# Optimization experiments

Hardware: AMD Instinct MI355X
Metric: run time of the kernel (lower is better)

Reference implementation:

```python
import jax, jax.numpy as jnp
import numpy as np


def setup_inputs() -> dict:
    key = jax.random.key(0)
    ks = jax.random.split(key, 10)
    B, S, V, E, C = 256, 512, 50000, 300, 10
    sentences = jax.random.randint(ks[0], (B, S), 0, V)
    emb_table = jax.random.normal(ks[1], (V, E), dtype=jnp.float32) * 0.1
    # pad_token=0 row zeroed like nn.Embedding(padding_idx=0)
    emb_table = emb_table.at[0].set(0.0)
    k3 = jax.random.normal(ks[2], (3, E), dtype=jnp.float32) * 0.05
    b3 = jax.random.normal(ks[3], (1,), dtype=jnp.float32) * 0.05
    k4 = jax.random.normal(ks[4], (4, E), dtype=jnp.float32) * 0.05
    b4 = jax.random.normal(ks[5], (1,), dtype=jnp.float32) * 0.05
    k5 = jax.random.normal(ks[6], (5, E), dtype=jnp.float32) * 0.05
    b5 = jax.random.normal(ks[7], (1,), dtype=jnp.float32) * 0.05
    fc_w = jax.random.normal(ks[8], (C, 3), dtype=jnp.float32) * 0.1
    fc_b = jax.random.normal(ks[9], (C,), dtype=jnp.float32) * 0.1
    return {"sentences": sentences, "emb_table": emb_table,
            "k3": k3, "b3": b3, "k4": k4, "b4": b4, "k5": k5, "b5": b5,
            "fc_w": fc_w, "fc_b": fc_b}


def _window_feature(emb, k, b):
    # emb: [B,S,E]; k: [w,E]; conv with 1 in/1 out channel spanning full E (VALID)
    out = jax.lax.conv_general_dilated(
        emb[:, None, :, :],            # [B,1,S,E]
        k[None, None, :, :],           # [1,1,w,E]
        window_strides=(1, 1), padding="VALID")  # [B,1,S-w+1,1]
    f = jnp.tanh(out[:, 0, :, 0] + b)  # [B,S-w+1]
    return f.max(axis=-1)              # [B]


def reference(sentences, emb_table, k3, b3, k4, b4, k5, b5, fc_w, fc_b):
    emb = emb_table[sentences]  # [B,S,E]
    feats = jnp.stack([_window_feature(emb, k3, b3),
                       _window_feature(emb, k4, b4),
                       _window_feature(emb, k5, b5)], axis=-1)  # [B,3]
    # dropout is identity in eval mode
    logits = feats @ fc_w.T + fc_b  # [B,C]
    return jax.nn.log_softmax(logits, axis=-1)
```

## Files before the change

### kernel.cpp

```cpp
#include <hip/hip_runtime.h>
#include <math.h>

#define NSENT 256
#define SLEN  512
#define VROWS 50000
#define EDIM  300
#define NC4   75
#define NROW  12

__global__ __launch_bounds__(256, 4)
void vocab_scores(const float* __restrict__ emb,
                  const float* __restrict__ k3,
                  const float* __restrict__ k4,
                  const float* __restrict__ k5,
                  float* __restrict__ s)
{
    __shared__ float part[4][64][13];
    __shared__ float red[64 * 13];

    const int lane  = threadIdx.x & 63;
    const int wave  = threadIdx.x >> 6;
    const int chunk = __builtin_amdgcn_readfirstlane(wave);

    const int v0 = blockIdx.x * 64;
    const int v  = min(v0 + lane, VROWS - 1);

    const float4* erow = reinterpret_cast<const float4*>(emb + (size_t)v * EDIM);
    const float4* k3v  = reinterpret_cast<const float4*>(k3);
    const float4* k4v  = reinterpret_cast<const float4*>(k4);
    const float4* k5v  = reinterpret_cast<const float4*>(k5);

    const int  c0   = chunk * 19;
    const bool full = (chunk < 3);

    float4 ev[18];
    #pragma unroll
    for (int i = 0; i < 18; ++i) ev[i] = erow[c0 + i];
    float4 evL;
    if (full) evL = erow[c0 + 18];

    float acc[NROW];
    #pragma unroll
    for (int r = 0; r < NROW; ++r) acc[r] = 0.f;

    auto fma_col = [&](const float4 ev_, int c) {
        #pragma unroll
        for (int r = 0; r < 3; ++r) {
            const float4 kv = k3v[r * NC4 + c];
            acc[r] = fmaf(ev_.x, kv.x, acc[r]);
            acc[r] = fmaf(ev_.y, kv.y, acc[r]);
            acc[r] = fmaf(ev_.z, kv.z, acc[r]);
            acc[r] = fmaf(ev_.w, kv.w, acc[r]);
        }
        #pragma unroll
        for (int r = 0; r < 4; ++r) {
            const float4 kv = k4v[r * NC4 + c];
            acc[3+r] = fmaf(ev_.x, kv.x, acc[3+r]);
            acc[3+r] = fmaf(ev_.y, kv.y, acc[3+r]);
            acc[3+r] = fmaf(ev_.z, kv.z, acc[3+r]);
            acc[3+r] = fmaf(ev_.w, kv.w, acc[3+r]);
        }
        #pragma unroll
        for (int r = 0; r < 5; ++r) {
            const float4 kv = k5v[r * NC4 + c];
            acc[7+r] = fmaf(ev_.x, kv.x, acc[7+r]);
            acc[7+r] = fmaf(ev_.y, kv.y, acc[7+r]);
            acc[7+r] = fmaf(ev_.z, kv.z, acc[7+r]);
            acc[7+r] = fmaf(ev_.w, kv.w, acc[7+r]);
        }
    };

    #pragma unroll
    for (int i = 0; i < 18; ++i) fma_col(ev[i], c0 + i);
    if (full) fma_col(evL, c0 + 18);

    #pragma unroll
    for (int r = 0; r < NROW; ++r) part[wave][lane][r] = acc[r];
    __syncthreads();

    const int r0 = wave * 3;
    #pragma unroll
    for (int rr = 0; rr < 3; ++rr) {
        const int r = r0 + rr;
        red[lane * 13 + r] = part[0][lane][r] + part[1][lane][r] +
                             part[2][lane][r] + part[3][lane][r];
    }
    __syncthreads();

    for (int j = threadIdx.x; j < 64 * NROW; j += 256) {
        const int gi = v0 * NROW + j;
        if (gi < VROWS * NROW)
            s[gi] = red[(j / NROW) * 13 + (j % NROW)];
    }
}

__global__ __launch_bounds__(1024, 1)
void textcnn_finish(const int*   __restrict__ sent,
                    const float* __restrict__ s,
                    const float* __restrict__ b3,
                    const float* __restrict__ b4,
                    const float* __restrict__ b5,
                    const float* __restrict__ fcw,
                    const float* __restrict__ fcb,
                    float* __restrict__ out)
{
    __shared__ float s_lds[NROW * SLEN];
    __shared__ float red[8][3];

    const int b = blockIdx.x;
    const int t = threadIdx.x;

    auto gather = [&](int token, int j) {
        const int widx = sent[b * SLEN + token];
        const float4 v = reinterpret_cast<const float4*>(s + (size_t)widx * NROW)[j];
        s_lds[(4*j + 0) * SLEN + token] = v.x;
        s_lds[(4*j + 1) * SLEN + token] = v.y;
        s_lds[(4*j + 2) * SLEN + token] = v.z;
        s_lds[(4*j + 3) * SLEN + token] = v.w;
    };

    gather(t & 511, t >> 9);
    if (t < SLEN) gather(t, 2);
    __syncthreads();

    if (t < SLEN) {
        const float bb3 = b3[0], bb4 = b4[0], bb5 = b5[0];
        float m3 = -1e30f, m4 = -1e30f, m5 = -1e30f;
        if (t < SLEN - 2)
            m3 = tanhf(s_lds[0*SLEN + t] + s_lds[1*SLEN + t+1] +
                       s_lds[2*SLEN + t+2] + bb3);
        if (t < SLEN - 3)
            m4 = tanhf(s_lds[3*SLEN + t] + s_lds[4*SLEN + t+1] +
                       s_lds[5*SLEN + t+2] + s_lds[6*SLEN + t+3] + bb4);
        if (t < SLEN - 4)
            m5 = tanhf(s_lds[7*SLEN + t] + s_lds[8*SLEN + t+1] +
                       s_lds[9*SLEN + t+2] + s_lds[10*SLEN + t+3] +
                       s_lds[11*SLEN + t+4] + bb5);

        #pragma unroll
        for (int off = 32; off; off >>= 1) {
            m3 = fmaxf(m3, __shfl_xor(m3, off));
            m4 = fmaxf(m4, __shfl_xor(m4, off));
            m5 = fmaxf(m5, __shfl_xor(m5, off));
        }
        if ((t & 63) == 0) {
            const int w = t >> 6;
            red[w][0] = m3; red[w][1] = m4; red[w][2] = m5;
        }
    }
    __syncthreads();

    if (t == 0) {
        float f3 = red[0][0], f4 = red[0][1], f5 = red[0][2];
        #pragma unroll
        for (int w = 1; w < 8; ++w) {
            f3 = fmaxf(f3, red[w][0]);
            f4 = fmaxf(f4, red[w][1]);
            f5 = fmaxf(f5, red[w][2]);
        }
        float lg[10];
        float mx = -1e30f;
        #pragma unroll
        for (int c = 0; c < 10; ++c) {
            lg[c] = fcb[c] + f3 * fcw[c*3+0] + f4 * fcw[c*3+1] + f5 * fcw[c*3+2];
            mx = fmaxf(mx, lg[c]);
        }
        float ssum = 0.f;
        #pragma unroll
        for (int c = 0; c < 10; ++c) ssum += expf(lg[c] - mx);
        const float lse = logf(ssum);
        #pragma unroll
        for (int c = 0; c < 10; ++c) out[b * 10 + c] = lg[c] - mx - lse;
    }
}

extern "C" void kernel_launch(void* const* d_in, const int* in_sizes, int n_in,
                              void* d_out, int out_size, void* d_ws, size_t ws_size,
                              hipStream_t stream) {
    const int*   sent = (const int*)  d_in[0];
    const float* emb  = (const float*)d_in[1];
    const float* k3   = (const float*)d_in[2];
    const float* b3   = (const float*)d_in[3];
    const float* k4   = (const float*)d_in[4];
    const float* b4   = (const float*)d_in[5];
    const float* k5   = (const float*)d_in[6];
    const float* b5   = (const float*)d_in[7];
    const float* fcw  = (const float*)d_in[8];
    const float* fcb  = (const float*)d_in[9];
    float* out = (float*)d_out;
    float* s   = (float*)d_ws;

    const int nblk = (VROWS + 63) / 64;
    vocab_scores<<<nblk, 256, 0, stream>>>(emb, k3, k4, k5, s);
    textcnn_finish<<<NSENT, 1024, 0, stream>>>(sent, s, b3, b4, b5, fcw, fcb, out);
}
```

Baseline: 28.44 us.

## Stage embedding tiles through LDS with coalesced loads and register prefetch

The vocab scoring kernel now loads each 64-row embedding tile with coalesced float4 loads across the whole block and writes it into a padded LDS buffer. Each lane then reads its row back from LDS for the dot products; before, every lane read its own row directly with strided global loads. Each block now handles two tiles, and the second tile's global loads are issued into registers before the first tile is computed, so the fetch overlaps the math. The cost is roughly 85KB of LDS per block and launch bounds of one block per CU, with half as many blocks. This lowers occupancy and may limit latency hiding on a memory-bound kernel.

```diff
diff --git a/kernel.cpp b/kernel.cpp
--- a/kernel.cpp
+++ b/kernel.cpp
@@ -7,91 +7,123 @@
 #define EDIM  300
 #define NC4   75
 #define NROW  12
-
-__global__ __launch_bounds__(256, 4)
+#define TROWS 64
+#define TF4   (TROWS * NC4)
+#define LDS_S4 77
+
+__global__ __launch_bounds__(256, 1)
 void vocab_scores(const float* __restrict__ emb,
                   const float* __restrict__ k3,
                   const float* __restrict__ k4,
                   const float* __restrict__ k5,
                   float* __restrict__ s)
 {
-    __shared__ float part[4][64][13];
-    __shared__ float red[64 * 13];
-
-    const int lane  = threadIdx.x & 63;
-    const int wave  = threadIdx.x >> 6;
+    __shared__ float4 ebuf[TROWS * LDS_S4];
+    __shared__ float  part[4][TROWS][13];
+    __shared__ float  red[TROWS * 13];
+
+    const int tid   = threadIdx.x;
+    const int lane  = tid & 63;
+    const int wave  = tid >> 6;
     const int chunk = __builtin_amdgcn_readfirstlane(wave);
-
-    const int v0 = blockIdx.x * 64;
-    const int v  = min(v0 + lane, VROWS - 1);
-
-    const float4* erow = reinterpret_cast<const float4*>(emb + (size_t)v * EDIM);
-    const float4* k3v  = reinterpret_cast<const float4*>(k3);
-    const float4* k4v  = reinterpret_cast<const float4*>(k4);
-    const float4* k5v  = reinterpret_cast<const float4*>(k5);
-
-    const int  c0   = chunk * 19;
+    const int c0    = chunk * 19;
     const bool full = (chunk < 3);
 
-    float4 ev[18];
-    #pragma unroll
-    for (int i = 0; i < 18; ++i) ev[i] = erow[c0 + i];
-    float4 evL;
-    if (full) evL = erow[c0 + 18];
-
-    float acc[NROW];
-    #pragma unroll
-    for (int r = 0; r < NROW; ++r) acc[r] = 0.f;
-
-    auto fma_col = [&](const float4 ev_, int c) {
+    const float4* embf4 = reinterpret_cast<const float4*>(emb);
+    const float4* k3v   = reinterpret_cast<const float4*>(k3);
+    const float4* k4v   = reinterpret_cast<const float4*>(k4);
+    const float4* k5v   = reinterpret_cast<const float4*>(k5);
+
+    const int row00 = blockIdx.x * (2 * TROWS);
+
+    float4 pre[19];
+
+    auto issue_loads = [&](int tile_row0) {
+        #pragma unroll
+        for (int k = 0; k < 19; ++k) {
+            const int g = k * 256 + tid;
+            float4 v = make_float4(0.f, 0.f, 0.f, 0.f);
+            if (g < TF4 && (tile_row0 + g / NC4) < VROWS)
+                v = embf4[tile_row0 * NC4 + g];
+            pre[k] = v;
+        }
+    };
+
+    auto write_lds = [&]() {
+        #pragma unroll
+        for (int k = 0; k < 19; ++k) {
+            const int g = k * 256 + tid;
+            if (g < TF4)
+                ebuf[(g / NC4) * LDS_S4 + (g % NC4)] = pre[k];
+        }
+    };
+
+    auto fma_col = [&](float acc[NROW], const float4 ev, int c) {
         #pragma unroll
         for (int r = 0; r < 3; ++r) {
             const float4 kv = k3v[r * NC4 + c];
-            acc[r] = fmaf(ev_.x, kv.x, acc[r]);
-            acc[r] = fmaf(ev_.y, kv.y, acc[r]);
-            acc[r] = fmaf(ev_.z, kv.z, acc[r]);
-            acc[r] = fmaf(ev_.w, kv.w, acc[r]);
+            acc[r] = fmaf(ev.x, kv.x, acc[r]);
+            acc[r] = fmaf(ev.y, kv.y, acc[r]);
+            acc[r] = fmaf(ev.z, kv.z, acc[r]);
+            acc[r] = fmaf(ev.w, kv.w, acc[r]);
         }
         #pragma unroll
         for (int r = 0; r < 4; ++r) {
             const float4 kv = k4v[r * NC4 + c];
-            acc[3+r] = fmaf(ev_.x, kv.x, acc[3+r]);
-            acc[3+r] = fmaf(ev_.y, kv.y, acc[3+r]);
-            acc[3+r] = fmaf(ev_.z, kv.z, acc[3+r]);
-            acc[3+r] = fmaf(ev_.w, kv.w, acc[3+r]);
+            acc[3+r] = fmaf(ev.x, kv.x, acc[3+r]);
+            acc[3+r] = fmaf(ev.y, kv.y, acc[3+r]);
+            acc[3+r] = fmaf(ev.z, kv.z, acc[3+r]);
+            acc[3+r] = fmaf(ev.w, kv.w, acc[3+r]);
         }
         #pragma unroll
         for (int r = 0; r < 5; ++r) {
             const float4 kv = k5v[r * NC4 + c];
-            acc[7+r] = fmaf(ev_.x, kv.x, acc[7+r]);
-            acc[7+r] = fmaf(ev_.y, kv.y, acc[7+r]);
-            acc[7+r] = fmaf(ev_.z, kv.z, acc[7+r]);
-            acc[7+r] = fmaf(ev_.w, kv.w, acc[7+r]);
-        }
-    };
-
-    #pragma unroll
-    for (int i = 0; i < 18; ++i) fma_col(ev[i], c0 + i);
-    if (full) fma_col(evL, c0 + 18);
-
-    #pragma unroll
-    for (int r = 0; r < NROW; ++r) part[wave][lane][r] = acc[r];
-    __syncthreads();
-
-    const int r0 = wave * 3;
-    #pragma unroll
-    for (int rr = 0; rr < 3; ++rr) {
-        const int r = r0 + rr;
-        red[lane * 13 + r] = part[0][lane][r] + part[1][lane][r] +
-                             part[2][lane][r] + part[3][lane][r];
-    }
-    __syncthreads();
-
-    for (int j = threadIdx.x; j < 64 * NROW; j += 256) {
-        const int gi = v0 * NROW + j;
-        if (gi < VROWS * NROW)
-            s[gi] = red[(j / NROW) * 13 + (j % NROW)];
-    }
+            acc[7+r] = fmaf(ev.x, kv.x, acc[7+r]);
+            acc[7+r] = fmaf(ev.y, kv.y, acc[7+r]);
+            acc[7+r] = fmaf(ev.z, kv.z, acc[7+r]);
+            acc[7+r] = fmaf(ev.w, kv.w, acc[7+r]);
+        }
+    };
+
+    auto compute_store = [&](int tile_row0) {
+        float acc[NROW];
+        #pragma unroll
+        for (int r = 0; r < NROW; ++r) acc[r] = 0.f;
+
+        #pragma unroll
+        for (int i = 0; i < 18; ++i)
+            fma_col(acc, ebuf[lane * LDS_S4 + c0 + i], c0 + i);
+        if (full)
+            fma_col(acc, ebuf[lane * LDS_S4 + c0 + 18], c0 + 18);
+
+        #pragma unroll
+        for (int r = 0; r < NROW; ++r) part[wave][lane][r] = acc[r];
+        __syncthreads();
+
+        const int r0 = wave * 3;
+        #pragma unroll
+        for (int rr = 0; rr < 3; ++rr) {
+            const int r = r0 + rr;
+            red[lane * 13 + r] = part[0][lane][r] + part[1][lane][r] +
+                                 part[2][lane][r] + part[3][lane][r];
+        }
+        __syncthreads();
+
+        for (int j = tid; j < TROWS * NROW; j += 256) {
+            const int gi = tile_row0 * NROW + j;
+            if (gi < VROWS * NROW)
+                s[gi] = red[(j / NROW) * 13 + (j % NROW)];
+        }
+    };
+
+    issue_loads(row00);
+    write_lds();
+    __syncthreads();
+    issue_loads(row00 + TROWS);
+    compute_store(row00);
+    write_lds();
+    __syncthreads();
+    compute_store(row00 + TROWS);
 }
 
 __global__ __launch_bounds__(1024, 1)
@@ -190,7 +222,7 @@
     float* out = (float*)d_out;
     float* s   = (float*)d_ws;
 
-    const int nblk = (VROWS + 63) / 64;
+    const int nblk = (VROWS + 2 * TROWS - 1) / (2 * TROWS);
     vocab_scores<<<nblk, 256, 0, stream>>>(emb, k3, k4, k5, s);
     textcnn_finish<<<NSENT, 1024, 0, stream>>>(sent, s, b3, b4, b5, fcw, fcb, out);
 }
```

Result: slower. 51.47 us (+81.0%).

## Compute vocab window scores with bf16 MFMA instead of scalar FMA

Applied to the files above, without the earlier changes.

Replaces the scalar FP32 dot-product kernel that computes per-vocab-row scores against the 12 conv kernel rows with a 16x16x32 bf16 MFMA formulation. Each wave handles 16 vocab rows and accumulates over K=320 in 10 steps, with the kernel weights held in registers as the B fragment. This removes the LDS cross-wave reduction and the two barriers. It trades FP32 accuracy for bf16 rounding of both embeddings and weights, which may perturb the max/tanh features. The kernel is likely bound by the 60MB embedding read, so the gain is uncertain.

```diff
diff --git a/kernel.cpp b/kernel.cpp
--- a/kernel.cpp
+++ b/kernel.cpp
@@ -1,96 +1,88 @@
 #include <hip/hip_runtime.h>
+#include <hip/hip_bf16.h>
 #include <math.h>
 
 #define NSENT 256
 #define SLEN  512
 #define VROWS 50000
 #define EDIM  300
-#define NC4   75
 #define NROW  12
+#define NSTEP 10
 
-__global__ __launch_bounds__(256, 4)
-void vocab_scores(const float* __restrict__ emb,
-                  const float* __restrict__ k3,
-                  const float* __restrict__ k4,
-                  const float* __restrict__ k5,
-                  float* __restrict__ s)
+typedef __attribute__((ext_vector_type(8))) short bf16x8;
+typedef __attribute__((ext_vector_type(4))) float f32x4;
+
+static __device__ __forceinline__ short f2bf(float f) {
+    __hip_bfloat16 h = __float2bfloat16(f);
+    short s;
+    __builtin_memcpy(&s, &h, sizeof(s));
+    return s;
+}
+
+__global__ __launch_bounds__(256, 2)
+void vocab_scores_mfma(const float* __restrict__ emb,
+                       const float* __restrict__ k3,
+                       const float* __restrict__ k4,
+                       const float* __restrict__ k5,
+                       float* __restrict__ s)
 {
-    __shared__ float part[4][64][13];
-    __shared__ float red[64 * 13];
+    const int lane = threadIdx.x & 63;
+    const int wave = threadIdx.x >> 6;
+    const int rc   = lane & 15;
+    const int kg   = lane >> 4;
 
-    const int lane  = threadIdx.x & 63;
-    const int wave  = threadIdx.x >> 6;
-    const int chunk = __builtin_amdgcn_readfirstlane(wave);
+    const int vbase = blockIdx.x * 64 + wave * 16;
+    const int vrow  = min(vbase + rc, VROWS - 1);
 
-    const int v0 = blockIdx.x * 64;
-    const int v  = min(v0 + lane, VROWS - 1);
+    const float* krow = nullptr;
+    if      (rc < 3)  krow = k3 + rc * EDIM;
+    else if (rc < 7)  krow = k4 + (rc - 3) * EDIM;
+    else if (rc < 12) krow = k5 + (rc - 7) * EDIM;
 
-    const float4* erow = reinterpret_cast<const float4*>(emb + (size_t)v * EDIM);
-    const float4* k3v  = reinterpret_cast<const float4*>(k3);
-    const float4* k4v  = reinterpret_cast<const float4*>(k4);
-    const float4* k5v  = reinterpret_cast<const float4*>(k5);
+    bf16x8 bfrag[NSTEP];
+    #pragma unroll
+    for (int st = 0; st < NSTEP; ++st) {
+        const int k0 = st * 32 + kg * 8;
+        float4 b0 = make_float4(0.f,0.f,0.f,0.f);
+        float4 b1 = make_float4(0.f,0.f,0.f,0.f);
+        if (krow) {
+            if (k0 + 4 <= EDIM) b0 = *reinterpret_cast<const float4*>(krow + k0);
+            if (k0 + 8 <= EDIM) b1 = *reinterpret_cast<const float4*>(krow + k0 + 4);
+        }
+        bf16x8 f;
+        f[0]=f2bf(b0.x); f[1]=f2bf(b0.y); f[2]=f2bf(b0.z); f[3]=f2bf(b0.w);
+        f[4]=f2bf(b1.x); f[5]=f2bf(b1.y); f[6]=f2bf(b1.z); f[7]=f2bf(b1.w);
+        bfrag[st] = f;
+    }
 
-    const int  c0   = chunk * 19;
-    const bool full = (chunk < 3);
+    const float* arow = emb + (size_t)vrow * EDIM;
+    float4 a0[NSTEP], a1[NSTEP];
+    #pragma unroll
+    for (int st = 0; st < NSTEP; ++st) {
+        const int k0 = st * 32 + kg * 8;
+        a0[st] = (k0 + 4 <= EDIM) ? *reinterpret_cast<const float4*>(arow + k0)
+                                  : make_float4(0.f,0.f,0.f,0.f);
+        a1[st] = (k0 + 8 <= EDIM) ? *reinterpret_cast<const float4*>(arow + k0 + 4)
+                                  : make_float4(0.f,0.f,0.f,0.f);
+    }
 
-    float4 ev[18];
+    f32x4 acc = {0.f, 0.f, 0.f, 0.f};
     #pragma unroll
-    for (int i = 0; i < 18; ++i) ev[i] = erow[c0 + i];
-    float4 evL;
-    if (full) evL = erow[c0 + 18];
+    for (int st = 0; st < NSTEP; ++st) {
+        bf16x8 af;
+        af[0]=f2bf(a0[st].x); af[1]=f2bf(a0[st].y);
+        af[2]=f2bf(a0[st].z); af[3]=f2bf(a0[st].w);
+        af[4]=f2bf(a1[st].x); af[5]=f2bf(a1[st].y);
+        af[6]=f2bf(a1[st].z); af[7]=f2bf(a1[st].w);
+        acc = __builtin_amdgcn_mfma_f32_16x16x32_bf16(af, bfrag[st], acc, 0, 0, 0);
+    }
 
-    float acc[NROW];
-    #pragma unroll
-    for (int r = 0; r < NROW; ++r) acc[r] = 0.f;
-
-    auto fma_col = [&](const float4 ev_, int c) {
+    if (rc < NROW) {
         #pragma unroll
-        for (int r = 0; r < 3; ++r) {
-            const float4 kv = k3v[r * NC4 + c];
-            acc[r] = fmaf(ev_.x, kv.x, acc[r]);
-            acc[r] = fmaf(ev_.y, kv.y, acc[r]);
-            acc[r] = fmaf(ev_.z, kv.z, acc[r]);
-            acc[r] = fmaf(ev_.w, kv.w, acc[r]);
+        for (int j = 0; j < 4; ++j) {
+            const int v = vbase + kg * 4 + j;
+            if (v < VROWS) s[(size_t)v * NROW + rc] = acc[j];
         }
-        #pragma unroll
-        for (int r = 0; r < 4; ++r) {
-            const float4 kv = k4v[r * NC4 + c];
-            acc[3+r] = fmaf(ev_.x, kv.x, acc[3+r]);
-            acc[3+r] = fmaf(ev_.y, kv.y, acc[3+r]);
-            acc[3+r] = fmaf(ev_.z, kv.z, acc[3+r]);
-            acc[3+r] = fmaf(ev_.w, kv.w, acc[3+r]);
-        }
-        #pragma unroll
-        for (int r = 0; r < 5; ++r) {
-            const float4 kv = k5v[r * NC4 + c];
-            acc[7+r] = fmaf(ev_.x, kv.x, acc[7+r]);
-            acc[7+r] = fmaf(ev_.y, kv.y, acc[7+r]);
-            acc[7+r] = fmaf(ev_.z, kv.z, acc[7+r]);
-            acc[7+r] = fmaf(ev_.w, kv.w, acc[7+r]);
-        }
-    };
-
-    #pragma unroll
-    for (int i = 0; i < 18; ++i) fma_col(ev[i], c0 + i);
-    if (full) fma_col(evL, c0 + 18);
-
-    #pragma unroll
-    for (int r = 0; r < NROW; ++r) part[wave][lane][r] = acc[r];
-    __syncthreads();
-
-    const int r0 = wave * 3;
-    #pragma unroll
-    for (int rr = 0; rr < 3; ++rr) {
-        const int r = r0 + rr;
-        red[lane * 13 + r] = part[0][lane][r] + part[1][lane][r] +
-                             part[2][lane][r] + part[3][lane][r];
-    }
-    __syncthreads();
-
-    for (int j = threadIdx.x; j < 64 * NROW; j += 256) {
-        const int gi = v0 * NROW + j;
-        if (gi < VROWS * NROW)
-            s[gi] = red[(j / NROW) * 13 + (j % NROW)];
     }
 }
 
@@ -191,6 +183,6 @@
     float* s   = (float*)d_ws;
 
     const int nblk = (VROWS + 63) / 64;
-    vocab_scores<<<nblk, 256, 0, stream>>>(emb, k3, k4, k5, s);
+    vocab_scores_mfma<<<nblk, 256, 0, stream>>>(emb, k3, k4, k5, s);
     textcnn_finish<<<NSENT, 1024, 0, stream>>>(sent, s, b3, b4, b5, fcw, fcb, out);
 }
```

New measurement: 28.98 us. Within noise of the previous version (+1.9%).
